# Kernel optimization log

Measured on AMD Instinct MI355X. Metric: run time of the kernel, lower is better.

## Reference

```python
import jax, jax.numpy as jnp
import numpy as np

N = 100_000   # atoms
B = 10_000    # building blocks
E = 320_000   # edges (bb <- atom)
D = 256       # embed_dim
H = 8         # heads
HD = D // H   # head_dim = 32
DIST = 64     # gaussian dist embed dim
MAX_R = 10.0


def setup_inputs() -> dict:
    key = jax.random.key(0)
    ks = jax.random.split(key, 10)
    atom_feats = jax.random.normal(ks[0], (N, D), jnp.float32)
    coords = jax.random.normal(ks[1], (N, 3), jnp.float32) * 3.0
    bb_vec = jnp.sort(jax.random.randint(ks[2], (N,), 0, B, jnp.int32))
    src = jax.random.randint(ks[3], (E,), 0, N, jnp.int32)
    tgt = jax.random.randint(ks[4], (E,), 0, B, jnp.int32)
    # linear params, [in, out] layout (x @ W + b)
    Wq = jax.random.normal(ks[5], (D, D), jnp.float32) / np.sqrt(D)
    Wk = jax.random.normal(ks[6], (D + DIST, D), jnp.float32) / np.sqrt(D + DIST)
    Wv = jax.random.normal(ks[7], (D + DIST, D), jnp.float32) / np.sqrt(D + DIST)
    Wo = jax.random.normal(ks[8], (D, D), jnp.float32) / np.sqrt(D)
    bq = jnp.zeros((D,), jnp.float32)
    bk = jnp.zeros((D,), jnp.float32)
    bv = jnp.zeros((D,), jnp.float32)
    bo = jnp.zeros((D,), jnp.float32)
    return dict(atom_feats=atom_feats, coords=coords, Wq=Wq, bq=bq, Wk=Wk, bk=bk,
                Wv=Wv, bv=bv, Wo=Wo, bo=bo, bb_vec=bb_vec, src=src, tgt=tgt)


def _gaussian_smearing(dist):
    offsets = jnp.linspace(0.0, MAX_R, DIST)            # [DIST]
    coeff = -0.5 / (offsets[1] - offsets[0]) ** 2
    return jnp.exp(coeff * (dist[:, None] - offsets) ** 2)  # [E, DIST]


def reference(atom_feats, coords, Wq, bq, Wk, bk, Wv, bv, Wo, bo, bb_vec, src, tgt):
    # building-block centers: mean coords, summed feats per bb
    counts = jax.ops.segment_sum(jnp.ones((N,), coords.dtype), bb_vec, num_segments=B)
    bb_center_pos = jax.ops.segment_sum(coords, bb_vec, num_segments=B)
    bb_center_pos = bb_center_pos / jnp.maximum(counts, 1.0)[:, None]       # [B, 3]
    bb_center_feats = jax.ops.segment_sum(atom_feats, bb_vec, num_segments=B)  # [B, D]

    # per-edge distance embedding
    edge_vec = coords[src] - bb_center_pos[tgt]                             # [E, 3]
    dist = jnp.sqrt(jnp.sum(edge_vec * edge_vec, axis=-1))                  # [E]
    edge_dist_embed = _gaussian_smearing(dist)                              # [E, DIST]

    # QKV
    q = (bb_center_feats @ Wq + bq).reshape(B, H, HD)                       # [B, H, HD]
    atom_input = jnp.concatenate([atom_feats[src], edge_dist_embed], -1)    # [E, D+DIST]
    k = (atom_input @ Wk + bk).reshape(E, H, HD)
    v = (atom_input @ Wv + bv).reshape(E, H, HD)

    # per-edge attention logits + segment softmax over tgt
    attn = jnp.einsum('ehc,ehc->eh', q[tgt], k) / np.sqrt(HD)               # [E, H]
    seg_max = jax.ops.segment_max(attn, tgt, num_segments=B)                # [B, H]
    ex = jnp.exp(attn - seg_max[tgt])
    denom = jax.ops.segment_sum(ex, tgt, num_segments=B)                    # [B, H]
    attn = ex / (denom[tgt] + 1e-16)

    # weighted scatter-sum of messages
    msg = attn[..., None] * v                                               # [E, H, HD]
    out = jax.ops.segment_sum(msg, tgt, num_segments=B).reshape(B, D)       # [B, D]
    return out @ Wo + bo
```

## Files before the change

### kernel.cpp

```cpp
#include <hip/hip_runtime.h>
#include <math.h>

#define N_ATOMS 100000
#define B_BB    10000
#define E_EDGES 320000
#define D_DIM   256
#define NHEAD   8
#define NDIST   64

#define DELTA   (10.0f/63.0f)
#define GCOEFF  (-0.5f/(DELTA*DELTA))
#define QKSCALE 0.17677669529663687f

__global__ void k_offsets(const int* __restrict__ bb_vec, int* __restrict__ atom_off,
                          int* __restrict__ edge_cnt) {
  int b = blockIdx.x * 256 + threadIdx.x;
  if (b <= B_BB) {
    int lo = 0, hi = N_ATOMS;
    while (lo < hi) { int mid = (lo + hi) >> 1; if (bb_vec[mid] < b) lo = mid + 1; else hi = mid; }
    atom_off[b] = lo;
  }
  if (b < B_BB) edge_cnt[b] = 0;
}

__global__ __launch_bounds__(256) void k_bb_centers(
    const float* __restrict__ af, const float* __restrict__ coords,
    const int* __restrict__ atom_off, float* __restrict__ bbF, float* __restrict__ bb_pos) {
  int t = threadIdx.x;
  for (int b = blockIdx.x; b < B_BB; b += gridDim.x) {
    int s = atom_off[b], e = atom_off[b + 1];
    float acc = 0.f;
    for (int a = s; a < e; a++) acc += af[(size_t)a * D_DIM + t];
    bbF[(size_t)b * D_DIM + t] = acc;
    if (t < 3) {
      float c = 0.f;
      for (int a = s; a < e; a++) c += coords[(size_t)a * 3 + t];
      float cnt = (float)(e - s);
      bb_pos[b * 4 + t] = c / fmaxf(cnt, 1.0f);
    }
  }
}

__global__ __launch_bounds__(256) void k_gemm256(
    const float* __restrict__ A, const float* __restrict__ W,
    const float* __restrict__ bias, float* __restrict__ C, int M) {
  __shared__ __align__(16) float As[16][68];
  __shared__ __align__(16) float Ws[16][64];
  int tid = threadIdx.x;
  int tx = tid & 15, ty = tid >> 4;
  int row0 = blockIdx.x * 64, col0 = blockIdx.y * 64;
  float acc[4][4] = {};
  for (int k0 = 0; k0 < 256; k0 += 16) {
    {
      int r = tid >> 2;
      int c = (tid & 3) * 4;
      int row = row0 + r;
      float4 v = make_float4(0.f, 0.f, 0.f, 0.f);
      if (row < M) v = *(const float4*)&A[(size_t)row * 256 + k0 + c];
      As[c + 0][r] = v.x; As[c + 1][r] = v.y; As[c + 2][r] = v.z; As[c + 3][r] = v.w;
    }
    {
      int r = tid >> 4;
      int c = (tid & 15) * 4;
      float4 v = *(const float4*)&W[(size_t)(k0 + r) * 256 + col0 + c];
      *(float4*)&Ws[r][c] = v;
    }
    __syncthreads();
#pragma unroll
    for (int kk = 0; kk < 16; kk++) {
      float4 a = *(const float4*)&As[kk][ty * 4];
      float4 b = *(const float4*)&Ws[kk][tx * 4];
      float av[4] = {a.x, a.y, a.z, a.w};
      float bv4[4] = {b.x, b.y, b.z, b.w};
#pragma unroll
      for (int i = 0; i < 4; i++)
#pragma unroll
        for (int j = 0; j < 4; j++) acc[i][j] += av[i] * bv4[j];
    }
    __syncthreads();
  }
#pragma unroll
  for (int i = 0; i < 4; i++) {
    int row = row0 + ty * 4 + i;
    if (row < M) {
      int col = col0 + tx * 4;
      float4 r = make_float4(acc[i][0] + bias[col + 0], acc[i][1] + bias[col + 1],
                             acc[i][2] + bias[col + 2], acc[i][3] + bias[col + 3]);
      *(float4*)&C[(size_t)row * 256 + col] = r;
    }
  }
}

__global__ void k_hist(const int* __restrict__ tgt, int* __restrict__ edge_cnt) {
  int e = blockIdx.x * 256 + threadIdx.x;
  if (e < E_EDGES) atomicAdd(&edge_cnt[tgt[e]], 1);
}

__global__ __launch_bounds__(1024) void k_scan(
    const int* __restrict__ edge_cnt, int* __restrict__ edge_start, int* __restrict__ cursor) {
  __shared__ int ssum[1024];
  int tid = threadIdx.x;
  int base = tid * 10;
  int v[10]; int s = 0;
#pragma unroll
  for (int k = 0; k < 10; k++) { int i = base + k; v[k] = (i < B_BB) ? edge_cnt[i] : 0; s += v[k]; }
  ssum[tid] = s;
  __syncthreads();
  for (int off = 1; off < 1024; off <<= 1) {
    int t = (tid >= off) ? ssum[tid - off] : 0;
    __syncthreads();
    ssum[tid] += t;
    __syncthreads();
  }
  int excl = ssum[tid] - s;
#pragma unroll
  for (int k = 0; k < 10; k++) {
    int i = base + k;
    if (i < B_BB) { edge_start[i] = excl; cursor[i] = excl; }
    excl += v[k];
  }
  if (tid == 1023) edge_start[B_BB] = E_EDGES;
}

__global__ void k_fill(const int* __restrict__ src, const int* __restrict__ tgt,
                       const float* __restrict__ coords, const float* __restrict__ bb_pos,
                       int* __restrict__ cursor, int* __restrict__ src_sorted,
                       float* __restrict__ dist_sorted) {
  int e = blockIdx.x * 256 + threadIdx.x;
  if (e >= E_EDGES) return;
  int b = tgt[e], a = src[e];
  int pos = atomicAdd(&cursor[b], 1);
  float dx = coords[a * 3 + 0] - bb_pos[b * 4 + 0];
  float dy = coords[a * 3 + 1] - bb_pos[b * 4 + 1];
  float dz = coords[a * 3 + 2] - bb_pos[b * 4 + 2];
  src_sorted[pos] = a;
  dist_sorted[pos] = sqrtf(dx * dx + dy * dy + dz * dz);
}

__global__ __launch_bounds__(256) void k_wt(
    const float* __restrict__ q, const float* __restrict__ Wk, float* __restrict__ wt) {
  __shared__ __align__(16) float As[32][132];
  __shared__ __align__(16) float Bs[32][68];
  int tid = threadIdx.x;
  int b0 = blockIdx.x * 128;
  int i0 = blockIdx.y * 64;
  int h  = blockIdx.z;
  {
    int r = tid >> 1, c0 = (tid & 1) * 16;
    int row = b0 + r;
    const float* qp = q + (size_t)row * 256 + h * 32 + c0;
#pragma unroll
    for (int jj = 0; jj < 4; ++jj) {
      float4 v = make_float4(0.f, 0.f, 0.f, 0.f);
      if (row < B_BB) v = *(const float4*)(qp + 4 * jj);
      As[c0 + 4*jj + 0][r] = v.x; As[c0 + 4*jj + 1][r] = v.y;
      As[c0 + 4*jj + 2][r] = v.z; As[c0 + 4*jj + 3][r] = v.w;
    }
  }
  {
    int r = tid >> 2, c0 = (tid & 3) * 8;
    const float* wp = Wk + (size_t)(i0 + r) * 256 + h * 32 + c0;
#pragma unroll
    for (int jj = 0; jj < 2; ++jj) {
      float4 v = *(const float4*)(wp + 4 * jj);
      Bs[c0 + 4*jj + 0][r] = v.x; Bs[c0 + 4*jj + 1][r] = v.y;
      Bs[c0 + 4*jj + 2][r] = v.z; Bs[c0 + 4*jj + 3][r] = v.w;
    }
  }
  __syncthreads();
  int tx = tid & 15, ty = tid >> 4;
  float acc[8][4] = {};
#pragma unroll
  for (int kk = 0; kk < 32; ++kk) {
    float4 a0 = *(const float4*)&As[kk][ty * 8];
    float4 a1 = *(const float4*)&As[kk][ty * 8 + 4];
    float4 b4 = *(const float4*)&Bs[kk][tx * 4];
    float av[8] = {a0.x, a0.y, a0.z, a0.w, a1.x, a1.y, a1.z, a1.w};
    float bv4[4] = {b4.x, b4.y, b4.z, b4.w};
#pragma unroll
    for (int i = 0; i < 8; ++i)
#pragma unroll
      for (int j = 0; j < 4; ++j) acc[i][j] += av[i] * bv4[j];
  }
#pragma unroll
  for (int i = 0; i < 8; ++i) {
    int row = b0 + ty * 8 + i;
    if (row < B_BB) {
      float4 o = make_float4(acc[i][0] * QKSCALE, acc[i][1] * QKSCALE,
                             acc[i][2] * QKSCALE, acc[i][3] * QKSCALE);
      *(float4*)&wt[(size_t)row * 2560 + h * 320 + i0 + tx * 4] = o;
    }
  }
}

__global__ __launch_bounds__(256) void k_attn(
    const float* __restrict__ af, float* __restrict__ wtS,
    const int* __restrict__ edge_start, const int* __restrict__ src_sorted,
    const float* __restrict__ dist_sorted, float* __restrict__ wsum) {
  int tid = threadIdx.x;
  int lane = tid & 63;
  int wv = tid >> 6;
  int h0 = 2 * wv, h1 = 2 * wv + 1;
  int g = lane >> 4;
  int sub = lane & 15;
  int b = blockIdx.x;

  int s0 = edge_start[b], e1 = edge_start[b + 1];
  float* wtb = wtS + (size_t)b * 2560;
  const float* wr0 = wtb + h0 * 320;
  const float* wr1 = wtb + h1 * 320;

  float W0[16], W1[16], wd0[4], wd1[4];
#pragma unroll
  for (int j = 0; j < 4; ++j) {
    float4 t0 = *(const float4*)(wr0 + sub * 16 + 4 * j);
    float4 t1 = *(const float4*)(wr1 + sub * 16 + 4 * j);
    W0[4*j+0] = t0.x; W0[4*j+1] = t0.y; W0[4*j+2] = t0.z; W0[4*j+3] = t0.w;
    W1[4*j+0] = t1.x; W1[4*j+1] = t1.y; W1[4*j+2] = t1.z; W1[4*j+3] = t1.w;
  }
#pragma unroll
  for (int j = 0; j < 4; ++j) { wd0[j] = wr0[256 + sub + 16*j]; wd1[j] = wr1[256 + sub + 16*j]; }

  float l0 = 0.f, l1 = 0.f;
  float S0r[16] = {}, S1r[16] = {};
  float sd0[4] = {}, sd1[4] = {};

  if (s0 < e1) {
    int e1m1 = e1 - 1;
    int i0 = min(s0 + g, e1m1);
    int aC = src_sorted[i0];
    float dC = dist_sorted[i0];
    int i1 = min(s0 + 4 + g, e1m1);
    int aN = src_sorted[i1];
    float dN = dist_sorted[i1];
    const float4* crow = (const float4*)(af + (size_t)aC * 256 + sub * 16);
    float4 A0 = crow[0], A1 = crow[1], A2 = crow[2], A3 = crow[3];

    for (int eb = s0; eb < e1; eb += 4) {
      int i2 = min(eb + 8 + g, e1m1);
      int aN2 = src_sorted[i2];
      float dN2 = dist_sorted[i2];
      const float4* nrow = (const float4*)(af + (size_t)aN * 256 + sub * 16);
      float4 P0 = nrow[0], P1 = nrow[1], P2 = nrow[2], P3 = nrow[3];

      float Ar[16];
      Ar[0]=A0.x; Ar[1]=A0.y; Ar[2]=A0.z; Ar[3]=A0.w;
      Ar[4]=A1.x; Ar[5]=A1.y; Ar[6]=A1.z; Ar[7]=A1.w;
      Ar[8]=A2.x; Ar[9]=A2.y; Ar[10]=A2.z; Ar[11]=A2.w;
      Ar[12]=A3.x; Ar[13]=A3.y; Ar[14]=A3.z; Ar[15]=A3.w;
      float emb[4];
#pragma unroll
      for (int j = 0; j < 4; ++j) {
        float dd = dC - (float)(sub + 16 * j) * DELTA;
        emb[j] = __expf(GCOEFF * dd * dd);
      }
      float p0 = 0.f, p1 = 0.f;
#pragma unroll
      for (int c = 0; c < 16; ++c) { p0 += Ar[c] * W0[c]; p1 += Ar[c] * W1[c]; }
#pragma unroll
      for (int j = 0; j < 4; ++j) { p0 += emb[j] * wd0[j]; p1 += emb[j] * wd1[j]; }
#pragma unroll
      for (int off = 8; off > 0; off >>= 1) {
        p0 += __shfl_xor(p0, off);
        p1 += __shfl_xor(p1, off);
      }
      float w0 = __expf(p0), w1 = __expf(p1);
      if (eb + g >= e1) { w0 = 0.f; w1 = 0.f; }
      l0 += w0; l1 += w1;
#pragma unroll
      for (int c = 0; c < 16; ++c) {
        S0r[c] = fmaf(w0, Ar[c], S0r[c]);
        S1r[c] = fmaf(w1, Ar[c], S1r[c]);
      }
#pragma unroll
      for (int j = 0; j < 4; ++j) {
        sd0[j] = fmaf(w0, emb[j], sd0[j]);
        sd1[j] = fmaf(w1, emb[j], sd1[j]);
      }

      A0 = P0; A1 = P1; A2 = P2; A3 = P3;
      dC = dN;
      aN = aN2; dN = dN2;
    }
  }

#pragma unroll
  for (int off = 16; off <= 32; off <<= 1) {
    l0 += __shfl_xor(l0, off);
    l1 += __shfl_xor(l1, off);
#pragma unroll
    for (int c = 0; c < 16; ++c) {
      S0r[c] += __shfl_xor(S0r[c], off);
      S1r[c] += __shfl_xor(S1r[c], off);
    }
#pragma unroll
    for (int j = 0; j < 4; ++j) {
      sd0[j] += __shfl_xor(sd0[j], off);
      sd1[j] += __shfl_xor(sd1[j], off);
    }
  }

  float inv0 = 1.0f / (l0 + 1e-16f), inv1 = 1.0f / (l1 + 1e-16f);
  if (g == 0) {
#pragma unroll
    for (int j = 0; j < 4; ++j) {
      float4 o0 = make_float4(S0r[4*j+0]*inv0, S0r[4*j+1]*inv0, S0r[4*j+2]*inv0, S0r[4*j+3]*inv0);
      float4 o1 = make_float4(S1r[4*j+0]*inv1, S1r[4*j+1]*inv1, S1r[4*j+2]*inv1, S1r[4*j+3]*inv1);
      *(float4*)(wtb + h0 * 320 + sub * 16 + 4 * j) = o0;
      *(float4*)(wtb + h1 * 320 + sub * 16 + 4 * j) = o1;
    }
#pragma unroll
    for (int j = 0; j < 4; ++j) {
      wtb[h0 * 320 + 256 + sub + 16 * j] = sd0[j] * inv0;
      wtb[h1 * 320 + 256 + sub + 16 * j] = sd1[j] * inv1;
    }
    if (sub == 0) {
      wsum[b * 8 + h0] = l0 * inv0;
      wsum[b * 8 + h1] = l1 * inv1;
    }
  }
}

__global__ __launch_bounds__(256) void k_out_head(
    const float* __restrict__ Sf, const float* __restrict__ Wv,
    const float* __restrict__ bv, const float* __restrict__ wsum,
    float* __restrict__ out_pre) {
  __shared__ __align__(16) float As[32][132];
  __shared__ __align__(16) float Bs[32][36];
  int tid = threadIdx.x;
  int b0 = blockIdx.x * 128;
  int h  = blockIdx.y;
  int tx = tid & 7, ty = tid >> 3;
  float acc[4][4] = {};
  for (int k0 = 0; k0 < 320; k0 += 32) {
    {
      int r = tid >> 1, c0 = (tid & 1) * 16;
      int row = b0 + r;
      const float* sp = Sf + (size_t)row * 2560 + h * 320 + k0 + c0;
#pragma unroll
      for (int jj = 0; jj < 4; ++jj) {
        float4 v = make_float4(0.f, 0.f, 0.f, 0.f);
        if (row < B_BB) v = *(const float4*)(sp + 4 * jj);
        As[c0 + 4*jj + 0][r] = v.x; As[c0 + 4*jj + 1][r] = v.y;
        As[c0 + 4*jj + 2][r] = v.z; As[c0 + 4*jj + 3][r] = v.w;
      }
    }
    {
      int r = tid >> 3, c0 = (tid & 7) * 4;
      float4 v = *(const float4*)&Wv[(size_t)(k0 + r) * 256 + h * 32 + c0];
      *(float4*)&Bs[r][c0] = v;
    }
    __syncthreads();
#pragma unroll
    for (int kk = 0; kk < 32; ++kk) {
      float4 a4 = *(const float4*)&As[kk][ty * 4];
      float4 b4 = *(const float4*)&Bs[kk][tx * 4];
      float av[4] = {a4.x, a4.y, a4.z, a4.w};
      float bv4[4] = {b4.x, b4.y, b4.z, b4.w};
#pragma unroll
      for (int i = 0; i < 4; ++i)
#pragma unroll
        for (int j = 0; j < 4; ++j) acc[i][j] += av[i] * bv4[j];
    }
    __syncthreads();
  }
  float bvv[4];
#pragma unroll
  for (int j = 0; j < 4; ++j) bvv[j] = bv[h * 32 + tx * 4 + j];
#pragma unroll
  for (int i = 0; i < 4; ++i) {
    int row = b0 + ty * 4 + i;
    if (row < B_BB) {
      float ws = wsum[row * 8 + h];
      float4 o = make_float4(acc[i][0] + ws * bvv[0], acc[i][1] + ws * bvv[1],
                             acc[i][2] + ws * bvv[2], acc[i][3] + ws * bvv[3]);
      *(float4*)&out_pre[(size_t)row * 256 + h * 32 + tx * 4] = o;
    }
  }
}

extern "C" void kernel_launch(void* const* d_in, const int* in_sizes, int n_in,
                              void* d_out, int out_size, void* d_ws, size_t ws_size,
                              hipStream_t stream) {
  const float* af     = (const float*)d_in[0];
  const float* coords = (const float*)d_in[1];
  const float* Wq     = (const float*)d_in[2];
  const float* bq     = (const float*)d_in[3];
  const float* Wk     = (const float*)d_in[4];
  const float* bk     = (const float*)d_in[5];  (void)bk;
  const float* Wv     = (const float*)d_in[6];
  const float* bv     = (const float*)d_in[7];
  const float* Wo     = (const float*)d_in[8];
  const float* bo     = (const float*)d_in[9];
  const int* bb_vec   = (const int*)d_in[10];
  const int* src      = (const int*)d_in[11];
  const int* tgt      = (const int*)d_in[12];
  float* out = (float*)d_out;
  (void)in_sizes; (void)n_in; (void)out_size; (void)ws_size;

  char* ws = (char*)d_ws;
  size_t o = 0;
  auto alloc = [&](size_t bytes) { size_t r = o; o += (bytes + 255) & ~(size_t)255; return r; };
  int*   atom_off    = (int*)(ws + alloc((B_BB + 1) * 4));
  int*   edge_cnt    = (int*)(ws + alloc((size_t)B_BB * 4));
  int*   edge_start  = (int*)(ws + alloc((B_BB + 1) * 4));
  int*   cursor      = (int*)(ws + alloc((size_t)B_BB * 4));
  int*   src_sorted  = (int*)(ws + alloc((size_t)E_EDGES * 4));
  float* dist_sorted = (float*)(ws + alloc((size_t)E_EDGES * 4));
  float* bbF         = (float*)(ws + alloc((size_t)B_BB * 256 * 4));
  float* bb_pos      = (float*)(ws + alloc((size_t)B_BB * 4 * 4));
  float* q           = (float*)(ws + alloc((size_t)B_BB * 256 * 4));
  float* wtS         = (float*)(ws + alloc((size_t)B_BB * 2560 * 4));
  float* wsum        = (float*)(ws + alloc((size_t)B_BB * 8 * 4));
  float* out_pre     = (float*)(ws + alloc((size_t)B_BB * 256 * 4));

  k_offsets<<<(B_BB + 1 + 255) / 256, 256, 0, stream>>>(bb_vec, atom_off, edge_cnt);
  k_bb_centers<<<2560, 256, 0, stream>>>(af, coords, atom_off, bbF, bb_pos);
  k_hist<<<(E_EDGES + 255) / 256, 256, 0, stream>>>(tgt, edge_cnt);
  k_scan<<<1, 1024, 0, stream>>>(edge_cnt, edge_start, cursor);
  k_fill<<<(E_EDGES + 255) / 256, 256, 0, stream>>>(src, tgt, coords, bb_pos, cursor,
                                                    src_sorted, dist_sorted);
  k_gemm256<<<dim3((B_BB + 63) / 64, 4), 256, 0, stream>>>(bbF, Wq, bq, q, B_BB);
  k_wt<<<dim3((B_BB + 127) / 128, 5, 8), 256, 0, stream>>>(q, Wk, wtS);
  k_attn<<<B_BB, 256, 0, stream>>>(af, wtS, edge_start, src_sorted, dist_sorted, wsum);
  k_out_head<<<dim3((B_BB + 127) / 128, 8), 256, 0, stream>>>(wtS, Wv, bv, wsum, out_pre);
  k_gemm256<<<dim3((B_BB + 63) / 64, 4), 256, 0, stream>>>(out_pre, Wo, bo, out, B_BB);
}
```

Measured before the change: 564.3 us.

## Split attention edge loop into logit and accumulation phases over 16-edge chunks

```diff
diff --git a/kernel.cpp b/kernel.cpp
--- a/kernel.cpp
+++ b/kernel.cpp
@@ -7,6 +7,7 @@
 #define D_DIM   256
 #define NHEAD   8
 #define NDIST   64
+#define EPAD    128
 
 #define DELTA   (10.0f/63.0f)
 #define GCOEFF  (-0.5f/(DELTA*DELTA))
@@ -97,7 +98,8 @@
 }
 
 __global__ __launch_bounds__(1024) void k_scan(
-    const int* __restrict__ edge_cnt, int* __restrict__ edge_start, int* __restrict__ cursor) {
+    const int* __restrict__ edge_cnt, int* __restrict__ edge_start, int* __restrict__ cursor,
+    int* __restrict__ src_sorted, float* __restrict__ dist_sorted) {
   __shared__ int ssum[1024];
   int tid = threadIdx.x;
   int base = tid * 10;
@@ -120,6 +122,7 @@
     excl += v[k];
   }
   if (tid == 1023) edge_start[B_BB] = E_EDGES;
+  if (tid < EPAD) { src_sorted[E_EDGES + tid] = 0; dist_sorted[E_EDGES + tid] = 0.f; }
 }
 
 __global__ void k_fill(const int* __restrict__ src, const int* __restrict__ tgt,
@@ -193,6 +196,14 @@
   }
 }
 
+#define FMA4(p, v, Wb, k) \
+  p = fmaf((v).x, Wb[(k)], p);   p = fmaf((v).y, Wb[(k)+1], p); \
+  p = fmaf((v).z, Wb[(k)+2], p); p = fmaf((v).w, Wb[(k)+3], p);
+
+#define ACC4(Sarr, k, ww, v) \
+  Sarr[(k)]   = fmaf(ww, (v).x, Sarr[(k)]);   Sarr[(k)+1] = fmaf(ww, (v).y, Sarr[(k)+1]); \
+  Sarr[(k)+2] = fmaf(ww, (v).z, Sarr[(k)+2]); Sarr[(k)+3] = fmaf(ww, (v).w, Sarr[(k)+3]);
+
 __global__ __launch_bounds__(256) void k_attn(
     const float* __restrict__ af, float* __restrict__ wtS,
     const int* __restrict__ edge_start, const int* __restrict__ src_sorted,
@@ -221,66 +232,75 @@
 #pragma unroll
   for (int j = 0; j < 4; ++j) { wd0[j] = wr0[256 + sub + 16*j]; wd1[j] = wr1[256 + sub + 16*j]; }
 
+  float cj[4];
+#pragma unroll
+  for (int j = 0; j < 4; ++j) cj[j] = (float)(sub + 16 * j) * DELTA;
+
   float l0 = 0.f, l1 = 0.f;
   float S0r[16] = {}, S1r[16] = {};
   float sd0[4] = {}, sd1[4] = {};
 
   if (s0 < e1) {
-    int e1m1 = e1 - 1;
-    int i0 = min(s0 + g, e1m1);
-    int aC = src_sorted[i0];
-    float dC = dist_sorted[i0];
-    int i1 = min(s0 + 4 + g, e1m1);
-    int aN = src_sorted[i1];
-    float dN = dist_sorted[i1];
+    int aC = src_sorted[s0 + g];
+    float dC = dist_sorted[s0 + g];
+    int aN = src_sorted[s0 + 4 + g];
+    float dN = dist_sorted[s0 + 4 + g];
     const float4* crow = (const float4*)(af + (size_t)aC * 256 + sub * 16);
     float4 A0 = crow[0], A1 = crow[1], A2 = crow[2], A3 = crow[3];
 
-    for (int eb = s0; eb < e1; eb += 4) {
-      int i2 = min(eb + 8 + g, e1m1);
-      int aN2 = src_sorted[i2];
-      float dN2 = dist_sorted[i2];
-      const float4* nrow = (const float4*)(af + (size_t)aN * 256 + sub * 16);
-      float4 P0 = nrow[0], P1 = nrow[1], P2 = nrow[2], P3 = nrow[3];
-
-      float Ar[16];
-      Ar[0]=A0.x; Ar[1]=A0.y; Ar[2]=A0.z; Ar[3]=A0.w;
-      Ar[4]=A1.x; Ar[5]=A1.y; Ar[6]=A1.z; Ar[7]=A1.w;
-      Ar[8]=A2.x; Ar[9]=A2.y; Ar[10]=A2.z; Ar[11]=A2.w;
-      Ar[12]=A3.x; Ar[13]=A3.y; Ar[14]=A3.z; Ar[15]=A3.w;
-      float emb[4];
-#pragma unroll
-      for (int j = 0; j < 4; ++j) {
-        float dd = dC - (float)(sub + 16 * j) * DELTA;
-        emb[j] = __expf(GCOEFF * dd * dd);
+    for (int cb = s0; cb < e1; cb += 16) {
+      float w0r[4], w1r[4];
+      int   a0r[4];
+#pragma unroll
+      for (int it = 0; it < 4; ++it) {
+        int eb = cb + 4 * it;
+        const float4* nrow = (const float4*)(af + (size_t)aN * 256 + sub * 16);
+        float4 P0 = nrow[0], P1 = nrow[1], P2 = nrow[2], P3 = nrow[3];
+        int i2 = eb + 8 + g;
+        int aN2 = src_sorted[i2];
+        float dN2 = dist_sorted[i2];
+
+        float emb[4];
+#pragma unroll
+        for (int j = 0; j < 4; ++j) {
+          float dd = dC - cj[j];
+          emb[j] = __expf(GCOEFF * dd * dd);
+        }
+        float p0 = 0.f, p1 = 0.f;
+        FMA4(p0, A0, W0, 0);  FMA4(p1, A0, W1, 0);
+        FMA4(p0, A1, W0, 4);  FMA4(p1, A1, W1, 4);
+        FMA4(p0, A2, W0, 8);  FMA4(p1, A2, W1, 8);
+        FMA4(p0, A3, W0, 12); FMA4(p1, A3, W1, 12);
+#pragma unroll
+        for (int j = 0; j < 4; ++j) { p0 = fmaf(emb[j], wd0[j], p0); p1 = fmaf(emb[j], wd1[j], p1); }
+#pragma unroll
+        for (int off = 8; off > 0; off >>= 1) {
+          p0 += __shfl_xor(p0, off);
+          p1 += __shfl_xor(p1, off);
+        }
+        float w0 = __expf(p0), w1 = __expf(p1);
+        if (eb + g >= e1) { w0 = 0.f; w1 = 0.f; }
+        l0 += w0; l1 += w1;
+#pragma unroll
+        for (int j = 0; j < 4; ++j) {
+          sd0[j] = fmaf(w0, emb[j], sd0[j]);
+          sd1[j] = fmaf(w1, emb[j], sd1[j]);
+        }
+        w0r[it] = w0; w1r[it] = w1; a0r[it] = aC;
+        A0 = P0; A1 = P1; A2 = P2; A3 = P3;
+        aC = aN; dC = dN;
+        aN = aN2; dN = dN2;
       }
-      float p0 = 0.f, p1 = 0.f;
-#pragma unroll
-      for (int c = 0; c < 16; ++c) { p0 += Ar[c] * W0[c]; p1 += Ar[c] * W1[c]; }
-#pragma unroll
-      for (int j = 0; j < 4; ++j) { p0 += emb[j] * wd0[j]; p1 += emb[j] * wd1[j]; }
-#pragma unroll
-      for (int off = 8; off > 0; off >>= 1) {
-        p0 += __shfl_xor(p0, off);
-        p1 += __shfl_xor(p1, off);
+#pragma unroll
+      for (int it = 0; it < 4; ++it) {
+        const float4* rrow = (const float4*)(af + (size_t)a0r[it] * 256 + sub * 16);
+        float4 R0 = rrow[0], R1 = rrow[1], R2 = rrow[2], R3 = rrow[3];
+        float w0 = w0r[it], w1 = w1r[it];
+        ACC4(S0r, 0,  w0, R0); ACC4(S1r, 0,  w1, R0);
+        ACC4(S0r, 4,  w0, R1); ACC4(S1r, 4,  w1, R1);
+        ACC4(S0r, 8,  w0, R2); ACC4(S1r, 8,  w1, R2);
+        ACC4(S0r, 12, w0, R3); ACC4(S1r, 12, w1, R3);
       }
-      float w0 = __expf(p0), w1 = __expf(p1);
-      if (eb + g >= e1) { w0 = 0.f; w1 = 0.f; }
-      l0 += w0; l1 += w1;
-#pragma unroll
-      for (int c = 0; c < 16; ++c) {
-        S0r[c] = fmaf(w0, Ar[c], S0r[c]);
-        S1r[c] = fmaf(w1, Ar[c], S1r[c]);
-      }
-#pragma unroll
-      for (int j = 0; j < 4; ++j) {
-        sd0[j] = fmaf(w0, emb[j], sd0[j]);
-        sd1[j] = fmaf(w1, emb[j], sd1[j]);
-      }
-
-      A0 = P0; A1 = P1; A2 = P2; A3 = P3;
-      dC = dN;
-      aN = aN2; dN = dN2;
     }
   }
 
@@ -405,8 +425,8 @@
   int*   edge_cnt    = (int*)(ws + alloc((size_t)B_BB * 4));
   int*   edge_start  = (int*)(ws + alloc((B_BB + 1) * 4));
   int*   cursor      = (int*)(ws + alloc((size_t)B_BB * 4));
-  int*   src_sorted  = (int*)(ws + alloc((size_t)E_EDGES * 4));
-  float* dist_sorted = (float*)(ws + alloc((size_t)E_EDGES * 4));
+  int*   src_sorted  = (int*)(ws + alloc((size_t)(E_EDGES + EPAD) * 4));
+  float* dist_sorted = (float*)(ws + alloc((size_t)(E_EDGES + EPAD) * 4));
   float* bbF         = (float*)(ws + alloc((size_t)B_BB * 256 * 4));
   float* bb_pos      = (float*)(ws + alloc((size_t)B_BB * 4 * 4));
   float* q           = (float*)(ws + alloc((size_t)B_BB * 256 * 4));
@@ -417,7 +437,7 @@
   k_offsets<<<(B_BB + 1 + 255) / 256, 256, 0, stream>>>(bb_vec, atom_off, edge_cnt);
   k_bb_centers<<<2560, 256, 0, stream>>>(af, coords, atom_off, bbF, bb_pos);
   k_hist<<<(E_EDGES + 255) / 256, 256, 0, stream>>>(tgt, edge_cnt);
-  k_scan<<<1, 1024, 0, stream>>>(edge_cnt, edge_start, cursor);
+  k_scan<<<1, 1024, 0, stream>>>(edge_cnt, edge_start, cursor, src_sorted, dist_sorted);
   k_fill<<<(E_EDGES + 255) / 256, 256, 0, stream>>>(src, tgt, coords, bb_pos, cursor,
                                                     src_sorted, dist_sorted);
   k_gemm256<<<dim3((B_BB + 63) / 64, 4), 256, 0, stream>>>(bbF, Wq, bq, q, B_BB);
```

New measurement: 642.8 us. 1.14x slower.
